# Performance work log

Hardware: AMD Instinct MI355X
Metric: run time of the kernel (lower is better)

The kernel has to match this reference:

```python
import jax, jax.numpy as jnp
import numpy as np

DEPTH = 6
D_IN = 512
D_OUT = 256
NUM_NODES = 2 ** (DEPTH + 1) - 1   # 127
NUM_LEAVES = 2 ** (DEPTH + 1)      # 128
BATCH = 8192
EPS = 0.01


def _routes(depth):
    num_nodes = 2 ** (depth + 1) - 1
    num_leaves = 2 ** (depth + 1)
    idxs = np.zeros((num_leaves, depth + 1), np.int32)
    sides = np.zeros((num_leaves, depth + 1), np.int32)
    for i in range(num_leaves):
        temp, temp_sides = [], []
        leaf_idx = num_nodes + i
        for _ in range(depth):
            parent_idx = (leaf_idx - 1) // 2
            temp.append(parent_idx)
            temp_sides.append(1 if (leaf_idx - 1) % 2 == 0 else 0)
            leaf_idx = parent_idx
        temp_sides.append(1 if (leaf_idx - 1) % 2 == 0 else 0)
        temp.append(0)
        idxs[i] = temp[::-1]
        sides[i] = temp_sides[::-1]
    return idxs, sides


def _l2norm(v, axis):
    # matches torch F.normalize (eps=1e-12)
    n = jnp.sqrt(jnp.sum(v * v, axis=axis, keepdims=True))
    return v / jnp.maximum(n, 1e-12)


def setup_inputs() -> dict:
    key = jax.random.key(0)
    ks = jax.random.split(key, 6)
    D1 = D_IN + 1  # pre-network output dim
    x = jax.random.normal(ks[0], (BATCH, D_IN), jnp.float32)
    # pre_network Linear(D_IN, D_IN+1)
    W_pre = jax.random.normal(ks[1], (D1, D_IN), jnp.float32) * (1.0 / np.sqrt(D_IN))
    b_pre = jax.random.normal(ks[2], (D1,), jnp.float32) * 0.01
    # node hyperplanes [num_nodes, D1]
    right_w = jax.random.normal(ks[3], (NUM_NODES, D1), jnp.float32)
    # leaves Linear(D1, out*num_leaves)
    W_leaf = jax.random.normal(ks[4], (D_OUT * NUM_LEAVES, D1), jnp.float32) * (1.0 / np.sqrt(D1))
    b_leaf = jax.random.normal(ks[5], (D_OUT * NUM_LEAVES,), jnp.float32) * 0.01
    idxs, sides = _routes(DEPTH)
    return {
        "x": x, "W_pre": W_pre, "b_pre": b_pre, "right_w": right_w,
        "W_leaf": W_leaf, "b_leaf": b_leaf,
        "route_idx": jnp.asarray(idxs, jnp.int32),
        "route_side": jnp.asarray(sides, jnp.int32),
    }


def reference(x, W_pre, b_pre, right_w, W_leaf, b_leaf, route_idx, route_side):
    b = x.shape[0]
    # pre-network: Linear + ReLU  -> [b, D1]
    h = jax.nn.relu(x @ W_pre.T + b_pre)
    # node probabilities (cosine-similarity routing)
    nx = _l2norm(h, axis=1)                  # [b, D1]
    nw = _l2norm(right_w, axis=1)            # [N, D1]
    right = nx @ nw.T                        # [b, N]
    right_dist = (1.0 - right) / 2.0
    left_dist = 1.0 - right_dist
    # all_indices [2, N, b]
    all_ind = jnp.stack([right_dist.T, left_dist.T], axis=0)
    # gather route probs -> [L, depth+1, b]
    probs = all_ind[route_side, route_idx]
    log_probs = jnp.log(jnp.clip(probs, EPS, 1.0 - EPS))
    leaves_logp = jnp.sum(log_probs, axis=1)        # [L, b]
    s_w = jnp.exp(leaves_logp)                       # [L, b]
    entropy = -jnp.sum(s_w * leaves_logp, axis=0)    # [b]
    max_entropy = (NUM_LEAVES / DEPTH) * jnp.log(jnp.float32(DEPTH))
    entropy_loss = entropy / max_entropy
    # all leaf outputs at once -> [b, L, out]
    results = (h @ W_leaf.T + b_leaf).reshape(b, NUM_LEAVES, D_OUT)
    # NOTE: original multiplies by (randn(1) + 1 + entropy_loss.mean());
    # the randn(1) term is fixed to 0 for a deterministic reference.
    scale = 1.0 + jnp.mean(entropy_loss)
    out = jnp.sum(results * scale * s_w.T[:, :, None], axis=1)  # [b, out]
    return out
```

## Files before the change

### kernel.cpp

```cpp
#include <hip/hip_runtime.h>

typedef _Float16 f16;
typedef unsigned short u16;
typedef unsigned int u32;
typedef _Float16 f16x8 __attribute__((ext_vector_type(8)));
typedef float f32x4 __attribute__((ext_vector_type(4)));
typedef float f32x16 __attribute__((ext_vector_type(16)));

union F16x8U { f16x8 v; uint4 q; u16 us[8]; f16 h[8]; };
union HBits { f16 f; u16 u; };

#define GLD16(g, l)                                                        \
  __builtin_amdgcn_global_load_lds(                                        \
      (const __attribute__((address_space(1))) void*)(g),                  \
      (__attribute__((address_space(3))) void*)(l), 16, 0, 0)

__global__ void kcvt_all(const float* __restrict__ x, f16* __restrict__ xo,
                         const float* __restrict__ w, f16* __restrict__ wo,
                         const float* __restrict__ rwsrc, f16* __restrict__ ro,
                         const float* __restrict__ wl, const float* __restrict__ blf,
                         f16* __restrict__ wpk) {
  int b = blockIdx.x;
  if (b < 2048) {
    int i = (b * 256 + threadIdx.x) << 3;
    float4 a = *(const float4*)(x + i);
    float4 c = *(const float4*)(x + i + 4);
    F16x8U u;
    u.h[0] = (f16)a.x; u.h[1] = (f16)a.y; u.h[2] = (f16)a.z; u.h[3] = (f16)a.w;
    u.h[4] = (f16)c.x; u.h[5] = (f16)c.y; u.h[6] = (f16)c.z; u.h[7] = (f16)c.w;
    *(uint4*)(xo + i) = u.q;
  } else if (b < 2336) {
    int e = ((b - 2048) * 256 + threadIdx.x) << 2;
    int row = e >> 9, col = e & 511;
    union { uint2 q; f16 h[4]; } u;
    if (row < 513) {
      float4 v = *(const float4*)(w + (size_t)row * 512 + col);
      u.h[0] = (f16)v.x; u.h[1] = (f16)v.y; u.h[2] = (f16)v.z; u.h[3] = (f16)v.w;
    } else {
      u.h[0] = u.h[1] = u.h[2] = u.h[3] = (f16)0.0f;
    }
    *(uint2*)(wo + e) = u.q;
  } else if (b < 2408) {
    int e = ((b - 2336) * 256 + threadIdx.x) << 2;
    int row = e / 576, c0 = e - row * 576;
    union { uint2 q; f16 h[4]; } u;
#pragma unroll
    for (int i = 0; i < 4; ++i) {
      int c = c0 + i;
      float v = (row < 127 && c < 513) ? rwsrc[(size_t)row * 513 + c] : 0.0f;
      u.h[i] = (f16)v;
    }
    *(uint2*)(ro + e) = u.q;
  } else {
    int e = ((b - 2408) * 256 + threadIdx.x) << 3;
    int row = e / 544, c0 = e - row * 544;
    const float* src = wl + (size_t)row * 513 + c0;
    F16x8U u;
#pragma unroll
    for (int i = 0; i < 8; ++i) {
      int c = c0 + i;
      float v = (c < 513) ? src[i] : ((c == 513) ? blf[row] : 0.0f);
      u.h[i] = (f16)v;
    }
    *(uint4*)(wpk + e) = u.q;
  }
}

template <int MODE>
__global__ __launch_bounds__(256, 2) void kgemm(
    const f16* __restrict__ A, const f16* __restrict__ B,
    const float* __restrict__ bias, void* __restrict__ C,
    int NK, int astr, int bstr) {
  __shared__ alignas(16) f16 al[2][128 * 32];
  __shared__ alignas(16) f16 bl[2][64 * 40];
  const int tid = threadIdx.x, lane = tid & 63, wid = tid >> 6;
  const int wm = wid >> 1, wn = wid & 1;
  const int brow = blockIdx.x << 7, bcol = blockIdx.y << 6;

  int arow[2], aseg[2];
#pragma unroll
  for (int i = 0; i < 2; ++i) { int c = i * 256 + tid; arow[i] = c >> 2; aseg[i] = c & 3; }
  int br0 = tid / 5, bs0 = tid - br0 * 5;
  int c1 = 256 + lane;
  int br1 = c1 / 5, bs1 = c1 - br1 * 5;

  f32x4 acc[4][2];
#pragma unroll
  for (int mf = 0; mf < 4; ++mf)
#pragma unroll
    for (int nf = 0; nf < 2; ++nf)
#pragma unroll
      for (int j = 0; j < 4; ++j) acc[mf][nf][j] = 0.0f;

  auto stage = [&](int kc, int bf) {
    int kcol = kc << 5;
#pragma unroll
    for (int i = 0; i < 2; ++i) {
      f16* ldsb = &al[bf][(i * 256 + (wid << 6)) << 3];
      GLD16(A + (size_t)(brow + arow[i]) * astr + kcol + (aseg[i] << 3), ldsb);
    }
    {
      f16* ldsb = &bl[bf][(wid << 6) << 3];
      GLD16(B + (size_t)(bcol + br0) * bstr + kcol + (bs0 < 4 ? (bs0 << 3) : 0), ldsb);
    }
    if (wid == 0) {
      f16* ldsb = &bl[bf][256 << 3];
      GLD16(B + (size_t)(bcol + br1) * bstr + kcol + (bs1 < 4 ? (bs1 << 3) : 0), ldsb);
    }
  };

  stage(0, 0);
  __syncthreads();
  int cur = 0;
  for (int kc = 0; kc < NK; ++kc) {
    if (kc + 1 < NK) stage(kc + 1, cur ^ 1);
    f16x8 af[4], bfm[2];
#pragma unroll
    for (int mf = 0; mf < 4; ++mf)
      af[mf] = *(const f16x8*)&al[cur][((wm << 6) + (mf << 4) + (lane & 15)) * 32 + ((lane >> 4) << 3)];
#pragma unroll
    for (int nf = 0; nf < 2; ++nf)
      bfm[nf] = *(const f16x8*)&bl[cur][((wn << 5) + (nf << 4) + (lane & 15)) * 40 + ((lane >> 4) << 3)];
#pragma unroll
    for (int mf = 0; mf < 4; ++mf)
#pragma unroll
      for (int nf = 0; nf < 2; ++nf)
        acc[mf][nf] = __builtin_amdgcn_mfma_f32_16x16x32_f16(af[mf], bfm[nf], acc[mf][nf], 0, 0, 0);
    __syncthreads();
    cur ^= 1;
  }

#pragma unroll
  for (int mf = 0; mf < 4; ++mf) {
#pragma unroll
    for (int nf = 0; nf < 2; ++nf) {
      int gcol = bcol + (wn << 5) + (nf << 4) + (lane & 15);
      int gr0 = brow + (wm << 6) + (mf << 4) + ((lane >> 4) << 2);
      if (MODE == 0) {
        float bv = (gcol < 513) ? bias[gcol] : 0.0f;
#pragma unroll
        for (int j = 0; j < 4; ++j) {
          float v = fmaxf(acc[mf][nf][j] + bv, 0.0f);
          ((f16*)C)[(size_t)(gr0 + j) * 576 + gcol] = (gcol == 513) ? (f16)1.0f : (f16)v;
        }
      } else {
#pragma unroll
        for (int j = 0; j < 4; ++j)
          ((float*)C)[(size_t)(gr0 + j) * 128 + gcol] = acc[mf][nf][j];
      }
    }
  }
}

__global__ void khnorm(const f16* __restrict__ hf, float* __restrict__ ihn) {
  int row = (blockIdx.x << 2) + (threadIdx.x >> 6);
  int lane = threadIdx.x & 63;
  float s = 0.0f;
  for (int c = lane; c < 513; c += 64) {
    float v = (float)hf[(size_t)row * 576 + c];
    s += v * v;
  }
  for (int o = 32; o; o >>= 1) s += __shfl_down(s, o);
  if (!lane) ihn[row] = 1.0f / fmaxf(sqrtf(s), 1e-12f);
}

__global__ void kinvrw(const float* __restrict__ rw, float* __restrict__ irw) {
  int j = (blockIdx.x << 2) + (threadIdx.x >> 6);
  if (j >= 127) return;
  int lane = threadIdx.x & 63;
  float s = 0.0f;
  for (int d = lane; d < 513; d += 64) {
    float v = rw[(size_t)j * 513 + d];
    s += v * v;
  }
  for (int o = 32; o; o >>= 1) s += __shfl_down(s, o);
  if (!lane) irw[j] = 1.0f / fmaxf(sqrtf(s), 1e-12f);
}

__global__ void kroute(const float* __restrict__ G, const float* __restrict__ ihn,
                       const float* __restrict__ irw, u16* __restrict__ swh,
                       float* __restrict__ entp) {
  int b = blockIdx.x * 256 + threadIdx.x;
  float ih = ihn[b];
  const float* g = G + (size_t)b * 128;
  float ent = 0.0f;
  size_t wbase = (size_t)(b & ~127) + (((b & 31) >> 1) << 3) + ((b & 1) << 2) + ((b >> 5) & 3);
  for (int l = 0; l < 128; ++l) {
    int n = 0;
    float lp = 0.0f;
#pragma unroll
    for (int k = 6; k >= 0; --k) {
      int bit = (l >> k) & 1;
      float cs = g[n] * ih * irw[n];
      float pr = bit ? 0.5f * (1.0f - cs) : 0.5f * (1.0f + cs);
      pr = fminf(fmaxf(pr, 0.01f), 0.99f);
      lp += __logf(pr);
      n = 2 * n + 1 + bit;
    }
    float sw = __expf(lp);
    ent -= sw * lp;
    HBits hb; hb.f = (f16)sw;
    swh[(size_t)l * 8192 + wbase] = hb.u;
  }
  for (int o = 32; o; o >>= 1) ent += __shfl_down(ent, o);
  __shared__ float red[4];
  if (!(threadIdx.x & 63)) red[threadIdx.x >> 6] = ent;
  __syncthreads();
  if (!threadIdx.x) atomicAdd(entp, red[0] + red[1] + red[2] + red[3]);
}

__global__ __launch_bounds__(512, 4) void kbig(
    const f16* __restrict__ hf, const f16* __restrict__ wp,
    const u16* __restrict__ swh, const float* __restrict__ entp,
    float* __restrict__ out) {
  __shared__ alignas(16) char smem[73728];

  const int tid = threadIdx.x, lane = tid & 63, wid = tid >> 6;
  const int obl = blockIdx.x & 7, mb = blockIdx.x >> 3;
  const int brow = mb << 7, ocol = obl << 5;

#pragma unroll
  for (int i = 0; i < 4; ++i) {
    int c = i * 512 + tid;
    int l = c >> 4, rg = c & 15;
    GLD16(swh + (size_t)l * 8192 + mb * 128 + rg * 8,
          smem + ((i * 512 + (wid << 6)) << 4));
  }
  auto stageA = [&](int kcp) {
    int c = tid & 255, q = c >> 7, row = c & 127;
    GLD16(hf + (size_t)(brow + row) * 576 + kcp * 16 + q * 8,
          smem + 65536 + ((kcp & 1) << 12) + ((wid & 3) << 10));
  };
  auto stageB = [&](int s2) {
    int kcp = s2 >> 4, lgp = s2 & 15;
    int col = lane & 31, q = (lane >> 5) & 1;
    GLD16(wp + (size_t)((lgp * 8 + wid) * 256 + ocol + col) * 544 + kcp * 16 + q * 8,
          smem + 32768 + ((s2 & 3) << 13) + (wid << 10));
  };
  stageA(0);
  stageB(0);
  stageB(1);

  f32x16 acc[4];
#pragma unroll
  for (int mf = 0; mf < 4; ++mf)
#pragma unroll
    for (int j = 0; j < 16; ++j) acc[mf][j] = 0.0f;

  f16x8 afr[4];
  const int aoff = 65536 + ((lane >> 5) << 11) + ((lane & 31) << 4);
  const int boff = 32768 + (wid << 10) + ((lane >> 5) << 9) + ((lane & 31) << 4);
  const int swoff = ((lane & 31) << 3);

  for (int kc = 0; kc < 33; ++kc) {
#pragma unroll
    for (int lg = 0; lg < 16; ++lg) {
      const int s = kc * 16 + lg;
      stageB(s + 2);
      if (lg == 4) stageA(kc + 1);
      if (lg >= 4 && lg <= 6) asm volatile("s_waitcnt vmcnt(3)" ::: "memory");
      else                    asm volatile("s_waitcnt vmcnt(2)" ::: "memory");
      __builtin_amdgcn_s_barrier();
      __builtin_amdgcn_sched_barrier(0);
      if (lg == 0) {
#pragma unroll
        for (int mf = 0; mf < 4; ++mf)
          afr[mf] = *(const f16x8*)(smem + aoff + ((kc & 1) << 12) + (mf << 9));
      }
      const int l = lg * 8 + wid;
      uint2 swq = *(const uint2*)(smem + (l << 8) + swoff);
      f16x8 bfr = *(const f16x8*)(smem + boff + ((s & 3) << 13));
      const u16* sc = (const u16*)&swq;
      __builtin_amdgcn_s_setprio(1);
#pragma unroll
      for (int mf = 0; mf < 4; ++mf) {
        HBits hb; hb.u = sc[mf];
        f16x8 as = afr[mf] * hb.f;
        acc[mf] = __builtin_amdgcn_mfma_f32_32x32x16_f16(as, bfr, acc[mf], 0, 0, 0);
      }
      __builtin_amdgcn_s_setprio(0);
      __builtin_amdgcn_sched_barrier(0);
    }
  }
  {
    const int kc = 33;
#pragma unroll
    for (int lg = 0; lg < 16; ++lg) {
      const int s = kc * 16 + lg;
      if (lg <= 13) stageB(s + 2);
      if (lg <= 13)      asm volatile("s_waitcnt vmcnt(2)" ::: "memory");
      else if (lg == 14) asm volatile("s_waitcnt vmcnt(1)" ::: "memory");
      else               asm volatile("s_waitcnt vmcnt(0)" ::: "memory");
      __builtin_amdgcn_s_barrier();
      __builtin_amdgcn_sched_barrier(0);
      if (lg == 0) {
#pragma unroll
        for (int mf = 0; mf < 4; ++mf)
          afr[mf] = *(const f16x8*)(smem + aoff + ((kc & 1) << 12) + (mf << 9));
      }
      const int l = lg * 8 + wid;
      uint2 swq = *(const uint2*)(smem + (l << 8) + swoff);
      f16x8 bfr = *(const f16x8*)(smem + boff + ((s & 3) << 13));
      const u16* sc = (const u16*)&swq;
      __builtin_amdgcn_s_setprio(1);
#pragma unroll
      for (int mf = 0; mf < 4; ++mf) {
        HBits hb; hb.u = sc[mf];
        f16x8 as = afr[mf] * hb.f;
        acc[mf] = __builtin_amdgcn_mfma_f32_32x32x16_f16(as, bfr, acc[mf], 0, 0, 0);
      }
      __builtin_amdgcn_s_setprio(0);
      __builtin_amdgcn_sched_barrier(0);
    }
  }

  auto writeAcc = [&](char* base) {
#pragma unroll
    for (int mf = 0; mf < 4; ++mf)
#pragma unroll
      for (int rq = 0; rq < 4; ++rq)
        *(f32x4*)(base + ((((mf << 2) + rq) << 6) + lane) * 16) =
            ((const f32x4*)&acc[mf])[rq];
  };
  auto addAcc = [&](const char* base) {
#pragma unroll
    for (int mf = 0; mf < 4; ++mf)
#pragma unroll
      for (int rq = 0; rq < 4; ++rq) {
        f32x4 v = *(const f32x4*)(base + ((((mf << 2) + rq) << 6) + lane) * 16);
        ((f32x4*)&acc[mf])[rq] += v;
      }
  };
  if (wid >= 4) writeAcc(smem + ((wid - 4) << 14));
  __syncthreads();
  if (wid < 4) addAcc(smem + (wid << 14));
  __syncthreads();
  if (wid == 2 || wid == 3) writeAcc(smem + ((wid - 2) << 14));
  __syncthreads();
  if (wid < 2) addAcc(smem + (wid << 14));
  __syncthreads();
  if (wid == 1) writeAcc(smem);
  __syncthreads();
  if (wid == 0) {
    addAcc(smem);
    float scale = 1.0f + (*entp) / (8192.0f * (128.0f / 6.0f) * logf(6.0f));
#pragma unroll
    for (int mf = 0; mf < 4; ++mf)
#pragma unroll
      for (int r = 0; r < 16; ++r) {
        int row = brow + (mf << 5) + (r & 3) + ((r >> 2) << 3) + ((lane >> 5) << 2);
        out[(size_t)row * 256 + ocol + (lane & 31)] = scale * acc[mf][r];
      }
  }
}

extern "C" void kernel_launch(void* const* d_in, const int* in_sizes, int n_in,
                              void* d_out, int out_size, void* d_ws, size_t ws_size,
                              hipStream_t stream) {
  const float* x     = (const float*)d_in[0];
  const float* wpre  = (const float*)d_in[1];
  const float* bpre  = (const float*)d_in[2];
  const float* rw    = (const float*)d_in[3];
  const float* wleaf = (const float*)d_in[4];
  const float* bleaf = (const float*)d_in[5];
  float* out = (float*)d_out;

  char* ws = (char*)d_ws;
  constexpr size_t O_ENT = 0;
  constexpr size_t O_XO  = 256;
  constexpr size_t O_WPO = O_XO  + 8388608;
  constexpr size_t O_RWO = O_WPO + 589824;
  constexpr size_t O_IRW = O_RWO + 147456;
  constexpr size_t O_HO  = O_IRW + 512;
  constexpr size_t O_IHN = O_HO  + 9437184;
  constexpr size_t O_G   = O_IHN + 32768;
  constexpr size_t O_SWH = O_G   + 4194304;
  constexpr size_t O_WPK = O_SWH + 2097152;

  float* ent = (float*)(ws + O_ENT);
  f16* xo   = (f16*)(ws + O_XO);
  f16* wpo  = (f16*)(ws + O_WPO);
  f16* rwo  = (f16*)(ws + O_RWO);
  float* irw = (float*)(ws + O_IRW);
  f16* ho   = (f16*)(ws + O_HO);
  float* ihn = (float*)(ws + O_IHN);
  float* go = (float*)(ws + O_G);
  u16* swh  = (u16*)(ws + O_SWH);
  f16* wpk  = (f16*)(ws + O_WPK);

  hipMemsetAsync(ent, 0, sizeof(float), stream);
  kcvt_all<<<11112, 256, 0, stream>>>(x, xo, wpre, wpo, rw, rwo, wleaf, bleaf, wpk);
  kgemm<0><<<dim3(64, 9), 256, 0, stream>>>(xo, wpo, bpre, (void*)ho, 16, 512, 512);
  khnorm<<<2048, 256, 0, stream>>>(ho, ihn);
  kinvrw<<<32, 256, 0, stream>>>(rw, irw);
  kgemm<1><<<dim3(64, 2), 256, 0, stream>>>(ho, rwo, nullptr, (void*)go, 17, 576, 576);
  kroute<<<32, 256, 0, stream>>>(go, ihn, irw, swh, ent);
  kbig<<<512, 512, 0, stream>>>(ho, wpk, swh, ent, out);
}
```

Baseline: 654.5 us.

## Halve kbig barriers by processing two B stages per sync; reuse route prefixes

The main leaf GEMM loop now handles two B stages (two leaf groups) per barrier, issuing two stage loads and eight MFMAs between syncs instead of one load and four. This halves the number of block-wide barriers and waitcnt points across the 34 k-chunks, and folds the tail into the main loop. kroute caches per-depth log-prob prefixes so only the changed suffix of each leaf path is recomputed, and it launches 64 blocks of 128 threads for more parallelism. The risks are deeper prefetch ordering with tighter buffer reuse in the 4-slot B ring, and higher register pressure.

Measured after the change: 583.1 us. 1.12x faster.

```diff
diff --git a/kernel.cpp b/kernel.cpp
--- a/kernel.cpp
+++ b/kernel.cpp
@@ -180,33 +180,37 @@
 __global__ void kroute(const float* __restrict__ G, const float* __restrict__ ihn,
                        const float* __restrict__ irw, u16* __restrict__ swh,
                        float* __restrict__ entp) {
-  int b = blockIdx.x * 256 + threadIdx.x;
+  int b = blockIdx.x * 128 + threadIdx.x;
   float ih = ihn[b];
   const float* g = G + (size_t)b * 128;
   float ent = 0.0f;
   size_t wbase = (size_t)(b & ~127) + (((b & 31) >> 1) << 3) + ((b & 1) << 2) + ((b >> 5) & 3);
+  float lp[8]; int nd[8];
+  nd[0] = 0; lp[0] = 0.0f;
   for (int l = 0; l < 128; ++l) {
-    int n = 0;
-    float lp = 0.0f;
-#pragma unroll
-    for (int k = 6; k >= 0; --k) {
-      int bit = (l >> k) & 1;
-      float cs = g[n] * ih * irw[n];
-      float pr = bit ? 0.5f * (1.0f - cs) : 0.5f * (1.0f + cs);
-      pr = fminf(fmaxf(pr, 0.01f), 0.99f);
-      lp += __logf(pr);
-      n = 2 * n + 1 + bit;
-    }
-    float sw = __expf(lp);
-    ent -= sw * lp;
+    int d0 = l ? (6 - __builtin_ctz(l)) : 0;
+#pragma unroll
+    for (int d = 0; d < 7; ++d) {
+      if (d >= d0) {
+        int n = nd[d];
+        int bit = (l >> (6 - d)) & 1;
+        float cs = g[n] * ih * irw[n];
+        float pr = bit ? 0.5f * (1.0f - cs) : 0.5f * (1.0f + cs);
+        pr = fminf(fmaxf(pr, 0.01f), 0.99f);
+        lp[d + 1] = lp[d] + __logf(pr);
+        nd[d + 1] = 2 * n + 1 + bit;
+      }
+    }
+    float sw = __expf(lp[7]);
+    ent -= sw * lp[7];
     HBits hb; hb.f = (f16)sw;
     swh[(size_t)l * 8192 + wbase] = hb.u;
   }
   for (int o = 32; o; o >>= 1) ent += __shfl_down(ent, o);
-  __shared__ float red[4];
+  __shared__ float red[2];
   if (!(threadIdx.x & 63)) red[threadIdx.x >> 6] = ent;
   __syncthreads();
-  if (!threadIdx.x) atomicAdd(entp, red[0] + red[1] + red[2] + red[3]);
+  if (!threadIdx.x) atomicAdd(entp, red[0] + red[1]);
 }
 
 __global__ __launch_bounds__(512, 4) void kbig(
@@ -249,71 +253,57 @@
 
   f16x8 afr[4];
   const int aoff = 65536 + ((lane >> 5) << 11) + ((lane & 31) << 4);
-  const int boff = 32768 + (wid << 10) + ((lane >> 5) << 9) + ((lane & 31) << 4);
-  const int swoff = ((lane & 31) << 3);
-
-  for (int kc = 0; kc < 33; ++kc) {
-#pragma unroll
-    for (int lg = 0; lg < 16; ++lg) {
-      const int s = kc * 16 + lg;
-      stageB(s + 2);
-      if (lg == 4) stageA(kc + 1);
-      if (lg >= 4 && lg <= 6) asm volatile("s_waitcnt vmcnt(3)" ::: "memory");
-      else                    asm volatile("s_waitcnt vmcnt(2)" ::: "memory");
+  const int boffc = 32768 + (wid << 10) + ((lane >> 5) << 9) + ((lane & 31) << 4);
+  const int swoff = (lane & 31) << 3;
+
+  for (int kc8 = 0; kc8 < 33; ++kc8) {
+    const bool tail = (kc8 == 32);
+#pragma unroll
+    for (int pp = 0; pp < 8; ++pp) {
+      const int p = kc8 * 8 + pp;
+      const int s0 = 2 * p;
+      if (!tail || pp < 7) { stageB(s0 + 2); stageB(s0 + 3); }
+      if (pp == 4 && !tail) stageA(kc8 + 1);
+      if (tail && pp == 7)         asm volatile("s_waitcnt vmcnt(0)" ::: "memory");
+      else if (pp == 4 || pp == 5) asm volatile("s_waitcnt vmcnt(3)" ::: "memory");
+      else                         asm volatile("s_waitcnt vmcnt(2)" ::: "memory");
       __builtin_amdgcn_s_barrier();
       __builtin_amdgcn_sched_barrier(0);
-      if (lg == 0) {
+      if (pp == 0) {
 #pragma unroll
         for (int mf = 0; mf < 4; ++mf)
-          afr[mf] = *(const f16x8*)(smem + aoff + ((kc & 1) << 12) + (mf << 9));
-      }
-      const int l = lg * 8 + wid;
-      uint2 swq = *(const uint2*)(smem + (l << 8) + swoff);
-      f16x8 bfr = *(const f16x8*)(smem + boff + ((s & 3) << 13));
-      const u16* sc = (const u16*)&swq;
+          afr[mf] = *(const f16x8*)(smem + aoff + ((kc8 & 1) << 12) + (mf << 9));
+      }
+      const int bufA = (pp & 1) << 1;
+      uint2 swqA = *(const uint2*)(smem + ((pp * 16 + wid) << 8) + swoff);
+      f16x8 bfA = *(const f16x8*)(smem + boffc + (bufA << 13));
+      uint2 swqB = *(const uint2*)(smem + ((pp * 16 + 8 + wid) << 8) + swoff);
+      f16x8 bfB = *(const f16x8*)(smem + boffc + ((bufA + 1) << 13));
       __builtin_amdgcn_s_setprio(1);
-#pragma unroll
-      for (int mf = 0; mf < 4; ++mf) {
-        HBits hb; hb.u = sc[mf];
-        f16x8 as = afr[mf] * hb.f;
-        acc[mf] = __builtin_amdgcn_mfma_f32_32x32x16_f16(as, bfr, acc[mf], 0, 0, 0);
+      {
+        const u16* sc = (const u16*)&swqA;
+#pragma unroll
+        for (int mf = 0; mf < 4; ++mf) {
+          HBits hb; hb.u = sc[mf];
+          f16x8 as = afr[mf] * hb.f;
+          acc[mf] = __builtin_amdgcn_mfma_f32_32x32x16_f16(as, bfA, acc[mf], 0, 0, 0);
+        }
+      }
+      {
+        const u16* sc = (const u16*)&swqB;
+#pragma unroll
+        for (int mf = 0; mf < 4; ++mf) {
+          HBits hb; hb.u = sc[mf];
+          f16x8 as = afr[mf] * hb.f;
+          acc[mf] = __builtin_amdgcn_mfma_f32_32x32x16_f16(as, bfB, acc[mf], 0, 0, 0);
+        }
       }
       __builtin_amdgcn_s_setprio(0);
       __builtin_amdgcn_sched_barrier(0);
     }
   }
-  {
-    const int kc = 33;
-#pragma unroll
-    for (int lg = 0; lg < 16; ++lg) {
-      const int s = kc * 16 + lg;
-      if (lg <= 13) stageB(s + 2);
-      if (lg <= 13)      asm volatile("s_waitcnt vmcnt(2)" ::: "memory");
-      else if (lg == 14) asm volatile("s_waitcnt vmcnt(1)" ::: "memory");
-      else               asm volatile("s_waitcnt vmcnt(0)" ::: "memory");
-      __builtin_amdgcn_s_barrier();
-      __builtin_amdgcn_sched_barrier(0);
-      if (lg == 0) {
-#pragma unroll
-        for (int mf = 0; mf < 4; ++mf)
-          afr[mf] = *(const f16x8*)(smem + aoff + ((kc & 1) << 12) + (mf << 9));
-      }
-      const int l = lg * 8 + wid;
-      uint2 swq = *(const uint2*)(smem + (l << 8) + swoff);
-      f16x8 bfr = *(const f16x8*)(smem + boff + ((s & 3) << 13));
-      const u16* sc = (const u16*)&swq;
-      __builtin_amdgcn_s_setprio(1);
-#pragma unroll
-      for (int mf = 0; mf < 4; ++mf) {
-        HBits hb; hb.u = sc[mf];
-        f16x8 as = afr[mf] * hb.f;
-        acc[mf] = __builtin_amdgcn_mfma_f32_32x32x16_f16(as, bfr, acc[mf], 0, 0, 0);
-      }
-      __builtin_amdgcn_s_setprio(0);
-      __builtin_amdgcn_sched_barrier(0);
-    }
-  }
-
+
+  __syncthreads();
   auto writeAcc = [&](char* base) {
 #pragma unroll
     for (int mf = 0; mf < 4; ++mf)
@@ -394,6 +384,6 @@
   khnorm<<<2048, 256, 0, stream>>>(ho, ihn);
   kinvrw<<<32, 256, 0, stream>>>(rw, irw);
   kgemm<1><<<dim3(64, 2), 256, 0, stream>>>(ho, rwo, nullptr, (void*)go, 17, 576, 576);
-  kroute<<<32, 256, 0, stream>>>(go, ihn, irw, swh, ent);
+  kroute<<<64, 128, 0, stream>>>(go, ihn, irw, swh, ent);
   kbig<<<512, 512, 0, stream>>>(ho, wpk, swh, ent, out);
 }
```
